# Kernel optimization log

Measured on AMD Instinct MI355X. Metric: run time of the kernel, lower is better.

The kernel has to match this reference:

```python
import jax, jax.numpy as jnp
import numpy as np

N = 100000
E = 3200000
D = 128
EPS = 1e-5


def setup_inputs() -> dict:
    key = jax.random.key(0)
    ks = jax.random.split(key, 9)
    h = jax.random.normal(ks[0], (N, D), dtype=jnp.float32)
    src = jax.random.randint(ks[1], (E,), 0, N, dtype=jnp.int64)
    dst = jax.random.randint(ks[2], (E,), 0, N, dtype=jnp.int64)
    s = 1.0 / np.sqrt(D)
    W_self = jax.random.uniform(ks[3], (D, D), jnp.float32, -s, s)
    W_neigh = jax.random.uniform(ks[4], (D, D), jnp.float32, -s, s)
    b = jax.random.uniform(ks[5], (D,), jnp.float32, -s, s)
    gamma = jnp.ones((D,), jnp.float32)
    beta = jnp.zeros((D,), jnp.float32)
    return {"h": h, "src": src, "dst": dst, "W_self": W_self,
            "W_neigh": W_neigh, "b": b, "gamma": gamma, "beta": beta}


def reference(h, src, dst, W_self, W_neigh, b, gamma, beta):
    # --- SAGEConv, mean aggregator (dropout p=0 -> identity) ---
    # gather source features along edges, segment-mean into destination nodes
    neigh_sum = jax.ops.segment_sum(h[src], dst, num_segments=N)      # [N, D]
    deg = jax.ops.segment_sum(jnp.ones((E,), h.dtype), dst, num_segments=N)
    neigh = neigh_sum / jnp.maximum(deg, 1.0)[:, None]                # [N, D]
    rst = h @ W_self + neigh @ W_neigh + b                            # [N, D]
    rst = jax.nn.relu(rst)                                            # activation
    # --- BatchNorm1d (training-mode batch statistics) ---
    mean = jnp.mean(rst, axis=0)
    var = jnp.var(rst, axis=0)
    rst = (rst - mean) * jax.lax.rsqrt(var + EPS) * gamma + beta
    # --- residual (in_feats == out_feats) ---
    return h + rst
```

## Files before the change

kernel.cpp:

```cpp
#include <hip/hip_runtime.h>

#define DCAP 2432
#define NBMAX 1600
#define SCATB 256
#define CONV2 512
#define WPB2 32
#define GB 1024
#define EORDCAP 3456

typedef __attribute__((ext_vector_type(2))) float f32x2;
typedef __attribute__((ext_vector_type(4))) float f32x4;
typedef __attribute__((ext_vector_type(8))) short bf16x8;

__device__ __forceinline__ unsigned short f2bf(float f) {
  union { float f; unsigned u; } c; c.f = f;
  unsigned u = c.u;
  unsigned r = u + 0x7FFFu + ((u >> 16) & 1u);
  return (unsigned short)(r >> 16);
}
__device__ __forceinline__ float bf2f(unsigned short s) {
  union { unsigned u; float f; } c; c.u = ((unsigned)s) << 16;
  return c.f;
}

__global__ __launch_bounds__(1024) void k_prescat(const float* __restrict__ h,
                                                  unsigned short* __restrict__ X,
                                                  unsigned* __restrict__ X8,
                                                  const float* __restrict__ Ws,
                                                  const float* __restrict__ Wn,
                                                  unsigned short* __restrict__ Wt,
                                                  const int* __restrict__ dst,
                                                  const int* __restrict__ src,
                                                  unsigned* __restrict__ esort,
                                                  int* __restrict__ gcur,
                                                  int nnodes, int E, int NB, int chunk) {
  __shared__ int cnt[NBMAX];
  __shared__ int gbase[NBMAX];
  int t = threadIdx.x;
  int bid = blockIdx.x;
  if (bid < SCATB) {
    int e0 = bid * chunk;
    int e1 = e0 + chunk; if (e1 > E) e1 = E;
    int n = e1 - e0;
    for (int i = t; i < NB; i += 1024) cnt[i] = 0;
    __syncthreads();
    for (int i = t; i < n; i += 1024)
      atomicAdd(&cnt[dst[e0 + i] >> 6], 1);
    __syncthreads();
    for (int bb = t; bb < NB; bb += 1024) {
      int len = cnt[bb];
      gbase[bb] = len ? atomicAdd(&gcur[bb], len) : 0;
      cnt[bb] = 0;
    }
    __syncthreads();
    for (int i = t; i < n; i += 1024) {
      int d = dst[e0 + i];
      int bb = d >> 6;
      int pos = gbase[bb] + atomicAdd(&cnt[bb], 1);
      if (pos < DCAP)
        esort[(long)bb * DCAP + pos] = ((unsigned)src[e0 + i] << 6) | (unsigned)(d & 63);
    }
  } else if (bid < SCATB + CONV2) {
    int stride = CONV2 * 1024;
    int total = nnodes * 32;
    for (int i = (bid - SCATB) * 1024 + t; i < total; i += stride) {
      int n = i >> 5, c = i & 31;
      float4 v = *(const float4*)(h + (long)n * 128 + c * 4);
      ushort4 o;
      o.x = f2bf(v.x); o.y = f2bf(v.y); o.z = f2bf(v.z); o.w = f2bf(v.w);
      *(ushort4*)(X + (long)n * 256 + c * 4) = o;
      int p8 = __builtin_amdgcn_cvt_pk_fp8_f32(v.x, v.y, 0, false);
      p8 = __builtin_amdgcn_cvt_pk_fp8_f32(v.z, v.w, p8, true);
      X8[(long)n * 32 + c] = (unsigned)p8;
    }
  } else if (bid < SCATB + CONV2 + WPB2) {
    int i = (bid - SCATB - CONV2) * 1024 + t;
    int col = i >> 8, k = i & 255;
    float v = (k < 128) ? Ws[k * 128 + col] : Wn[(k - 128) * 128 + col];
    Wt[col * 256 + k] = f2bf(v);
  } else {
    if (t < 32) X8[(long)nnodes * 32 + t] = 0u;
  }
}

__global__ __launch_bounds__(512) void k_aggb(unsigned short* __restrict__ X,
                                              const unsigned char* __restrict__ X8,
                                              const unsigned* __restrict__ esort,
                                              const int* __restrict__ gcur,
                                              int nnodes) {
  __shared__ unsigned eord[EORDCAP];
  __shared__ int dcnt[64], dstart[64], dcur[64], sc[64];
  int t = threadIdx.x;
  int b = blockIdx.x;
  int cntE = gcur[b]; if (cntE > DCAP) cntE = DCAP;
  const unsigned* ep = esort + (long)b * DCAP;
  if (t < 64) dcnt[t] = 0;
  __syncthreads();
  for (int i = t; i < cntE; i += 512)
    atomicAdd(&dcnt[ep[i] & 63u], 1);
  __syncthreads();
  int plen_t = 0;
  if (t < 64) { plen_t = (dcnt[t] + 15) & ~15; sc[t] = plen_t; }
  __syncthreads();
  for (int off = 1; off < 64; off <<= 1) {
    int v = (t < 64 && t >= off) ? sc[t - off] : 0;
    __syncthreads();
    if (t < 64) sc[t] += v;
    __syncthreads();
  }
  if (t < 64) { int ex = sc[t] - plen_t; dstart[t] = ex; dcur[t] = ex; }
  __syncthreads();
  int tot = sc[63];
  for (int i = t; i < tot; i += 512) eord[i] = (unsigned)nnodes;
  __syncthreads();
  for (int i = t; i < cntE; i += 512) {
    unsigned e = ep[i];
    int pos = atomicAdd(&dcur[e & 63u], 1);
    eord[pos] = e >> 6;
  }
  __syncthreads();

  int lane = t & 63, w = t >> 6;
  int qt = lane >> 4, ql = lane & 15;
  int ndst = nnodes - b * 64; if (ndst > 64) ndst = 64;
  for (int dl = w; dl < ndst; dl += 8) {
    int start = dstart[dl], dn = dcnt[dl];
    int plen = (dn + 15) & ~15;
    f32x2 acc[2][4];
#pragma unroll
    for (int u = 0; u < 2; u++)
#pragma unroll
      for (int j = 0; j < 4; j++) { acc[u][j].x = 0.f; acc[u][j].y = 0.f; }
    int i = 0;
    for (; i + 32 <= plen; i += 32) {
      uint2 v[8];
#pragma unroll
      for (int u = 0; u < 8; u++) {
        unsigned e = eord[start + i + u * 4 + qt];
        v[u] = *(const uint2*)(X8 + e * 128u + ql * 8u);
      }
#pragma unroll
      for (int u = 0; u < 8; u++) {
        acc[u & 1][0] += __builtin_amdgcn_cvt_pk_f32_fp8(v[u].x, false);
        acc[u & 1][1] += __builtin_amdgcn_cvt_pk_f32_fp8(v[u].x, true);
        acc[u & 1][2] += __builtin_amdgcn_cvt_pk_f32_fp8(v[u].y, false);
        acc[u & 1][3] += __builtin_amdgcn_cvt_pk_f32_fp8(v[u].y, true);
      }
    }
    if (i < plen) {
      uint2 v[4];
#pragma unroll
      for (int u = 0; u < 4; u++) {
        unsigned e = eord[start + i + u * 4 + qt];
        v[u] = *(const uint2*)(X8 + e * 128u + ql * 8u);
      }
#pragma unroll
      for (int u = 0; u < 4; u++) {
        acc[u & 1][0] += __builtin_amdgcn_cvt_pk_f32_fp8(v[u].x, false);
        acc[u & 1][1] += __builtin_amdgcn_cvt_pk_f32_fp8(v[u].x, true);
        acc[u & 1][2] += __builtin_amdgcn_cvt_pk_f32_fp8(v[u].y, false);
        acc[u & 1][3] += __builtin_amdgcn_cvt_pk_f32_fp8(v[u].y, true);
      }
    }
    float s[8];
#pragma unroll
    for (int j = 0; j < 4; j++) {
      s[2 * j] = acc[0][j].x + acc[1][j].x;
      s[2 * j + 1] = acc[0][j].y + acc[1][j].y;
    }
#pragma unroll
    for (int j = 0; j < 8; j++) {
      s[j] += __shfl_down(s[j], 32);
      s[j] += __shfl_down(s[j], 16);
    }
    if (qt == 0) {
      float scl = 1.0f / fmaxf((float)dn, 1.0f);
      uint4 o;
      o.x = (unsigned)f2bf(s[0] * scl) | ((unsigned)f2bf(s[1] * scl) << 16);
      o.y = (unsigned)f2bf(s[2] * scl) | ((unsigned)f2bf(s[3] * scl) << 16);
      o.z = (unsigned)f2bf(s[4] * scl) | ((unsigned)f2bf(s[5] * scl) << 16);
      o.w = (unsigned)f2bf(s[6] * scl) | ((unsigned)f2bf(s[7] * scl) << 16);
      *(uint4*)(X + (long)(b * 64 + dl) * 256 + 128 + ql * 8) = o;
    }
  }
}

__global__ __launch_bounds__(256) void k_gemm(const unsigned short* __restrict__ X,
                                              const unsigned short* __restrict__ Wt,
                                              const float* __restrict__ bias,
                                              unsigned short* __restrict__ rst8,
                                              float* __restrict__ psumA,
                                              float* __restrict__ psqA,
                                              int nnodes, int ntiles) {
  int t = threadIdx.x;
  int w = t >> 6, lane = t & 63;
  int m = lane & 15, q = lane >> 4;
  int col0 = w * 32 + m;
  int col1 = col0 + 16;
  bf16x8 b0[8], b1[8];
#pragma unroll
  for (int ks = 0; ks < 8; ks++) {
    b0[ks] = *(const bf16x8*)(Wt + col0 * 256 + q * 8 + ks * 32);
    b1[ks] = *(const bf16x8*)(Wt + col1 * 256 + q * 8 + ks * 32);
  }
  float bv0 = bias[col0], bv1 = bias[col1];
  float s0 = 0.f, sq0 = 0.f, s1 = 0.f, sq1 = 0.f;

#define LOADA(dst_, tb_)                                              \
  {                                                                   \
    int rowm_ = (tb_) * 16 + m;                                       \
    if (rowm_ >= nnodes) rowm_ = nnodes - 1;                          \
    const unsigned short* xp_ = X + (long)rowm_ * 256 + q * 8;        \
    _Pragma("unroll")                                                 \
    for (int ks = 0; ks < 8; ks++) dst_[ks] = *(const bf16x8*)(xp_ + ks * 32); \
  }

#define COMPUTE(a_, tb_)                                              \
  {                                                                   \
    f32x4 acc0 = {0.f, 0.f, 0.f, 0.f};                                \
    f32x4 acc1 = {0.f, 0.f, 0.f, 0.f};                                \
    _Pragma("unroll")                                                 \
    for (int ks = 0; ks < 8; ks++) {                                  \
      acc0 = __builtin_amdgcn_mfma_f32_16x16x32_bf16(a_[ks], b0[ks], acc0, 0, 0, 0); \
      acc1 = __builtin_amdgcn_mfma_f32_16x16x32_bf16(a_[ks], b1[ks], acc1, 0, 0, 0); \
    }                                                                 \
    _Pragma("unroll")                                                 \
    for (int r = 0; r < 4; r++) {                                     \
      int row = (tb_) * 16 + q * 4 + r;                               \
      if (row < nnodes) {                                             \
        float v0 = acc0[r] + bv0; v0 = v0 > 0.f ? v0 : 0.f;           \
        float v1 = acc1[r] + bv1; v1 = v1 > 0.f ? v1 : 0.f;           \
        rst8[(long)row * 128 + col0] = f2bf(v0);                      \
        rst8[(long)row * 128 + col1] = f2bf(v1);                      \
        s0 += v0; sq0 += v0 * v0;                                     \
        s1 += v1; sq1 += v1 * v1;                                     \
      }                                                               \
    }                                                                 \
  }

  int tb = blockIdx.x;
  if (tb < ntiles) {
    bf16x8 aA[8], aB[8];
    LOADA(aA, tb);
    for (; tb < ntiles; tb += 2 * GB) {
      int tb1 = tb + GB;
      if (tb1 < ntiles) LOADA(aB, tb1);
      COMPUTE(aA, tb);
      if (tb1 < ntiles) {
        int tb2 = tb1 + GB;
        if (tb2 < ntiles) LOADA(aA, tb2);
        COMPUTE(aB, tb1);
      }
    }
  }
#undef LOADA
#undef COMPUTE

  s0 += __shfl_down(s0, 32);  s0 += __shfl_down(s0, 16);
  sq0 += __shfl_down(sq0, 32); sq0 += __shfl_down(sq0, 16);
  s1 += __shfl_down(s1, 32);  s1 += __shfl_down(s1, 16);
  sq1 += __shfl_down(sq1, 32); sq1 += __shfl_down(sq1, 16);
  if (lane < 16) {
    atomicAdd(&psumA[col0], s0);
    atomicAdd(&psumA[col1], s1);
    atomicAdd(&psqA[col0], sq0);
    atomicAdd(&psqA[col1], sq1);
  }
}

__global__ void k_final(const unsigned short* __restrict__ X,
                        float* __restrict__ out,
                        const unsigned short* __restrict__ rst8,
                        const float* __restrict__ psumA,
                        const float* __restrict__ psqA,
                        const float* __restrict__ gamma,
                        const float* __restrict__ beta,
                        int nnodes, float Nf) {
  __shared__ float sc_s[128], sh_s[128];
  int t = threadIdx.x;
  if (t < 128) {
    float s = psumA[t], s2 = psqA[t];
    float mean = s / Nf;
    float var = s2 / Nf - mean * mean;
    float inv = rsqrtf(var + 1e-5f);
    float scv = gamma[t] * inv;
    sc_s[t] = scv;
    sh_s[t] = beta[t] - mean * scv;
  }
  __syncthreads();
  long stride = (long)gridDim.x * blockDim.x;
  long total = (long)nnodes * 16;
  for (long i = (long)blockIdx.x * blockDim.x + t; i < total; i += stride) {
    int c = (int)(i & 15);
    long row = i >> 4;
    uint4 rv = *(const uint4*)(rst8 + i * 8);
    uint4 hv = *(const uint4*)(X + row * 256 + c * 8);
    float4 sc0 = *(const float4*)(sc_s + c * 8);
    float4 sc1 = *(const float4*)(sc_s + c * 8 + 4);
    float4 sh0 = *(const float4*)(sh_s + c * 8);
    float4 sh1 = *(const float4*)(sh_s + c * 8 + 4);
    float4 o0, o1;
    o0.x = bf2f((unsigned short)(hv.x & 0xFFFFu)) + bf2f((unsigned short)(rv.x & 0xFFFFu)) * sc0.x + sh0.x;
    o0.y = bf2f((unsigned short)(hv.x >> 16))     + bf2f((unsigned short)(rv.x >> 16)) * sc0.y + sh0.y;
    o0.z = bf2f((unsigned short)(hv.y & 0xFFFFu)) + bf2f((unsigned short)(rv.y & 0xFFFFu)) * sc0.z + sh0.z;
    o0.w = bf2f((unsigned short)(hv.y >> 16))     + bf2f((unsigned short)(rv.y >> 16)) * sc0.w + sh0.w;
    o1.x = bf2f((unsigned short)(hv.z & 0xFFFFu)) + bf2f((unsigned short)(rv.z & 0xFFFFu)) * sc1.x + sh1.x;
    o1.y = bf2f((unsigned short)(hv.z >> 16))     + bf2f((unsigned short)(rv.z >> 16)) * sc1.y + sh1.y;
    o1.z = bf2f((unsigned short)(hv.w & 0xFFFFu)) + bf2f((unsigned short)(rv.w & 0xFFFFu)) * sc1.z + sh1.z;
    o1.w = bf2f((unsigned short)(hv.w >> 16))     + bf2f((unsigned short)(rv.w >> 16)) * sc1.w + sh1.w;
    *(float4*)(out + i * 8) = o0;
    *(float4*)(out + i * 8 + 4) = o1;
  }
}

extern "C" void kernel_launch(void* const* d_in, const int* in_sizes, int n_in,
                              void* d_out, int out_size, void* d_ws, size_t ws_size,
                              hipStream_t stream) {
  const float* h     = (const float*)d_in[0];
  const int*   src   = (const int*)d_in[1];
  const int*   dst   = (const int*)d_in[2];
  const float* Ws    = (const float*)d_in[3];
  const float* Wn    = (const float*)d_in[4];
  const float* bias  = (const float*)d_in[5];
  const float* gamma = (const float*)d_in[6];
  const float* beta  = (const float*)d_in[7];
  float* out = (float*)d_out;

  int nnodes = in_sizes[0] / 128;
  int E = in_sizes[1];
  int NB = (nnodes + 63) >> 6;
  int ntiles = (nnodes + 15) >> 4;
  int chunk = (E + SCATB - 1) / SCATB;

  char* ws = (char*)d_ws;
  size_t off = 0;
  unsigned short* X = (unsigned short*)(ws + off); off += (size_t)nnodes * 256 * 2;
  size_t off_alias = off;
  unsigned* X8 = (unsigned*)(ws + off);            off += (size_t)(nnodes + 1) * 128;
  unsigned* esort = (unsigned*)(ws + off);         off += (size_t)NB * DCAP * 4;
  unsigned short* rst8 = (unsigned short*)(ws + off_alias);
  unsigned short* Wt = (unsigned short*)(ws + off); off += 128 * 256 * 2;
  int* gcur = (int*)(ws + off);                    off += (size_t)NBMAX * 4;
  float* psumA = (float*)(ws + off);               off += 512;
  float* psqA = (float*)(ws + off);                off += 512;

  hipMemsetAsync(gcur, 0, (size_t)NBMAX * 4 + 1024, stream);
  k_prescat<<<SCATB + CONV2 + WPB2 + 1, 1024, 0, stream>>>(
      h, X, X8, Ws, Wn, Wt, dst, src, esort, gcur, nnodes, E, NB, chunk);
  k_aggb<<<NB, 512, 0, stream>>>(X, (const unsigned char*)X8, esort, gcur, nnodes);
  k_gemm<<<GB, 256, 0, stream>>>(X, Wt, bias, rst8, psumA, psqA, nnodes, ntiles);
  k_final<<<4096, 256, 0, stream>>>(X, out, rst8, psumA, psqA, gamma, beta,
                                    nnodes, (float)nnodes);
}
```

Before: 291.2 us.

## Replace global-atomic edge bucketing with per-chunk local sort and LDS-staged GEMM

Each scatter block now prefix-sums its local bucket counts. It writes edges into its own contiguous chunk of esort and records per-bucket counts and offsets in matrices, which removes the global atomic cursors and the memset. The aggregation block, now 256 threads, gathers its bucket's segments from all 256 chunks into LDS via a scan. The GEMM stages A tiles through a swizzled, double-buffered LDS tile instead of per-lane strided global loads. The cost is a serial, uncoalesced per-thread segment copy in aggregation, plus extra barriers and LDS use.

```diff
diff --git a/kernel.cpp b/kernel.cpp
--- a/kernel.cpp
+++ b/kernel.cpp
@@ -32,10 +32,12 @@
                                                   const int* __restrict__ dst,
                                                   const int* __restrict__ src,
                                                   unsigned* __restrict__ esort,
-                                                  int* __restrict__ gcur,
+                                                  int* __restrict__ cnt_mat,
+                                                  int* __restrict__ lofs_mat,
+                                                  float* __restrict__ psumA,
                                                   int nnodes, int E, int NB, int chunk) {
   __shared__ int cnt[NBMAX];
-  __shared__ int gbase[NBMAX];
+  __shared__ int tsum[1024];
   int t = threadIdx.x;
   int bid = blockIdx.x;
   if (bid < SCATB) {
@@ -47,18 +49,30 @@
     for (int i = t; i < n; i += 1024)
       atomicAdd(&cnt[dst[e0 + i] >> 6], 1);
     __syncthreads();
-    for (int bb = t; bb < NB; bb += 1024) {
-      int len = cnt[bb];
-      gbase[bb] = len ? atomicAdd(&gcur[bb], len) : 0;
-      cnt[bb] = 0;
+    int b0 = 2 * t, b1 = 2 * t + 1;
+    int c0 = (b0 < NB) ? cnt[b0] : 0;
+    int c1 = (b1 < NB) ? cnt[b1] : 0;
+    tsum[t] = c0 + c1;
+    __syncthreads();
+    for (int off = 1; off < 1024; off <<= 1) {
+      int v = (t >= off) ? tsum[t - off] : 0;
+      __syncthreads();
+      tsum[t] += v;
+      __syncthreads();
+    }
+    int ex = tsum[t] - (c0 + c1);
+    if (b0 < NB) {
+      *(int2*)&cnt_mat[(long)bid * NBMAX + b0] = make_int2(c0, c1);
+      *(int2*)&lofs_mat[(long)bid * NBMAX + b0] = make_int2(ex, ex + c0);
+      cnt[b0] = ex;
+      if (b1 < NB) cnt[b1] = ex + c0;
     }
     __syncthreads();
     for (int i = t; i < n; i += 1024) {
       int d = dst[e0 + i];
       int bb = d >> 6;
-      int pos = gbase[bb] + atomicAdd(&cnt[bb], 1);
-      if (pos < DCAP)
-        esort[(long)bb * DCAP + pos] = ((unsigned)src[e0 + i] << 6) | (unsigned)(d & 63);
+      int p = atomicAdd(&cnt[bb], 1);
+      esort[e0 + p] = ((unsigned)src[e0 + i] << 6) | (unsigned)(d & 63);
     }
   } else if (bid < SCATB + CONV2) {
     int stride = CONV2 * 1024;
@@ -80,24 +94,43 @@
     Wt[col * 256 + k] = f2bf(v);
   } else {
     if (t < 32) X8[(long)nnodes * 32 + t] = 0u;
-  }
-}
-
-__global__ __launch_bounds__(512) void k_aggb(unsigned short* __restrict__ X,
+    if (t >= 64 && t < 320) psumA[t - 64] = 0.f;
+  }
+}
+
+__global__ __launch_bounds__(256) void k_aggb(unsigned short* __restrict__ X,
                                               const unsigned char* __restrict__ X8,
                                               const unsigned* __restrict__ esort,
-                                              const int* __restrict__ gcur,
-                                              int nnodes) {
+                                              const int* __restrict__ cnt_mat,
+                                              const int* __restrict__ lofs_mat,
+                                              int nnodes, int chunk) {
+  __shared__ unsigned eload[DCAP];
   __shared__ unsigned eord[EORDCAP];
+  __shared__ int sseg[256];
   __shared__ int dcnt[64], dstart[64], dcur[64], sc[64];
   int t = threadIdx.x;
   int b = blockIdx.x;
-  int cntE = gcur[b]; if (cntE > DCAP) cntE = DCAP;
-  const unsigned* ep = esort + (long)b * DCAP;
+  int len = cnt_mat[(long)t * NBMAX + b];
+  int lof = lofs_mat[(long)t * NBMAX + b];
+  sseg[t] = len;
+  __syncthreads();
+  for (int off = 1; off < 256; off <<= 1) {
+    int v = (t >= off) ? sseg[t - off] : 0;
+    __syncthreads();
+    sseg[t] += v;
+    __syncthreads();
+  }
+  int dsto = sseg[t] - len;
+  int cntE = sseg[255]; if (cntE > DCAP) cntE = DCAP;
+  const unsigned* sp = esort + (long)t * chunk + lof;
+  for (int j = 0; j < len; j++) {
+    int di = dsto + j;
+    if (di < DCAP) eload[di] = sp[j];
+  }
   if (t < 64) dcnt[t] = 0;
   __syncthreads();
-  for (int i = t; i < cntE; i += 512)
-    atomicAdd(&dcnt[ep[i] & 63u], 1);
+  for (int i = t; i < cntE; i += 256)
+    atomicAdd(&dcnt[eload[i] & 63u], 1);
   __syncthreads();
   int plen_t = 0;
   if (t < 64) { plen_t = (dcnt[t] + 15) & ~15; sc[t] = plen_t; }
@@ -111,10 +144,10 @@
   if (t < 64) { int ex = sc[t] - plen_t; dstart[t] = ex; dcur[t] = ex; }
   __syncthreads();
   int tot = sc[63];
-  for (int i = t; i < tot; i += 512) eord[i] = (unsigned)nnodes;
-  __syncthreads();
-  for (int i = t; i < cntE; i += 512) {
-    unsigned e = ep[i];
+  for (int i = t; i < tot; i += 256) eord[i] = (unsigned)nnodes;
+  __syncthreads();
+  for (int i = t; i < cntE; i += 256) {
+    unsigned e = eload[i];
     int pos = atomicAdd(&dcur[e & 63u], 1);
     eord[pos] = e >> 6;
   }
@@ -123,7 +156,7 @@
   int lane = t & 63, w = t >> 6;
   int qt = lane >> 4, ql = lane & 15;
   int ndst = nnodes - b * 64; if (ndst > 64) ndst = 64;
-  for (int dl = w; dl < ndst; dl += 8) {
+  for (int dl = w; dl < ndst; dl += 4) {
     int start = dstart[dl], dn = dcnt[dl];
     int plen = (dn + 15) & ~15;
     f32x2 acc[2][4];
@@ -192,6 +225,7 @@
                                               float* __restrict__ psumA,
                                               float* __restrict__ psqA,
                                               int nnodes, int ntiles) {
+  __shared__ unsigned short atile[2][16][256];
   int t = threadIdx.x;
   int w = t >> 6, lane = t & 63;
   int m = lane & 15, q = lane >> 4;
@@ -206,55 +240,53 @@
   float bv0 = bias[col0], bv1 = bias[col1];
   float s0 = 0.f, sq0 = 0.f, s1 = 0.f, sq1 = 0.f;
 
-#define LOADA(dst_, tb_)                                              \
-  {                                                                   \
-    int rowm_ = (tb_) * 16 + m;                                       \
-    if (rowm_ >= nnodes) rowm_ = nnodes - 1;                          \
-    const unsigned short* xp_ = X + (long)rowm_ * 256 + q * 8;        \
-    _Pragma("unroll")                                                 \
-    for (int ks = 0; ks < 8; ks++) dst_[ks] = *(const bf16x8*)(xp_ + ks * 32); \
-  }
-
-#define COMPUTE(a_, tb_)                                              \
-  {                                                                   \
-    f32x4 acc0 = {0.f, 0.f, 0.f, 0.f};                                \
-    f32x4 acc1 = {0.f, 0.f, 0.f, 0.f};                                \
-    _Pragma("unroll")                                                 \
-    for (int ks = 0; ks < 8; ks++) {                                  \
-      acc0 = __builtin_amdgcn_mfma_f32_16x16x32_bf16(a_[ks], b0[ks], acc0, 0, 0, 0); \
-      acc1 = __builtin_amdgcn_mfma_f32_16x16x32_bf16(a_[ks], b1[ks], acc1, 0, 0, 0); \
-    }                                                                 \
-    _Pragma("unroll")                                                 \
-    for (int r = 0; r < 4; r++) {                                     \
-      int row = (tb_) * 16 + q * 4 + r;                               \
-      if (row < nnodes) {                                             \
-        float v0 = acc0[r] + bv0; v0 = v0 > 0.f ? v0 : 0.f;           \
-        float v1 = acc1[r] + bv1; v1 = v1 > 0.f ? v1 : 0.f;           \
-        rst8[(long)row * 128 + col0] = f2bf(v0);                      \
-        rst8[(long)row * 128 + col1] = f2bf(v1);                      \
-        s0 += v0; sq0 += v0 * v0;                                     \
-        s1 += v1; sq1 += v1 * v1;                                     \
-      }                                                               \
-    }                                                                 \
+#define STAGE(bufi, tb_)                                                        \
+  {                                                                             \
+    int r_ = t >> 4;                                                            \
+    long row_ = (long)(tb_) * 16 + r_;                                          \
+    if (row_ >= nnodes) row_ = nnodes - 1;                                      \
+    const unsigned short* gp_ = X + row_ * 256 + (t & 15) * 16;                 \
+    uint4 d0_ = *(const uint4*)gp_;                                             \
+    uint4 d1_ = *(const uint4*)(gp_ + 8);                                       \
+    int bo_ = (t & 15) * 32;                                                    \
+    char* lb_ = (char*)&atile[bufi][0][0] + r_ * 512;                           \
+    *(uint4*)(lb_ + (bo_ ^ ((r_ & 7) << 4))) = d0_;                             \
+    *(uint4*)(lb_ + ((bo_ + 16) ^ ((r_ & 7) << 4))) = d1_;                      \
   }
 
   int tb = blockIdx.x;
-  if (tb < ntiles) {
-    bf16x8 aA[8], aB[8];
-    LOADA(aA, tb);
-    for (; tb < ntiles; tb += 2 * GB) {
-      int tb1 = tb + GB;
-      if (tb1 < ntiles) LOADA(aB, tb1);
-      COMPUTE(aA, tb);
-      if (tb1 < ntiles) {
-        int tb2 = tb1 + GB;
-        if (tb2 < ntiles) LOADA(aA, tb2);
-        COMPUTE(aB, tb1);
-      }
-    }
-  }
-#undef LOADA
-#undef COMPUTE
+  int it = 0;
+  if (tb < ntiles) STAGE(0, tb);
+  for (; tb < ntiles; tb += GB, ++it) {
+    __syncthreads();
+    const char* lb = (const char*)&atile[it & 1][0][0] + m * 512;
+    bf16x8 a[8];
+#pragma unroll
+    for (int ks = 0; ks < 8; ks++)
+      a[ks] = *(const bf16x8*)(lb + ((q * 16 + ks * 64) ^ ((m & 7) << 4)));
+    int tbn = tb + GB;
+    if (tbn < ntiles) STAGE((it + 1) & 1, tbn);
+    f32x4 acc0 = {0.f, 0.f, 0.f, 0.f};
+    f32x4 acc1 = {0.f, 0.f, 0.f, 0.f};
+#pragma unroll
+    for (int ks = 0; ks < 8; ks++) {
+      acc0 = __builtin_amdgcn_mfma_f32_16x16x32_bf16(a[ks], b0[ks], acc0, 0, 0, 0);
+      acc1 = __builtin_amdgcn_mfma_f32_16x16x32_bf16(a[ks], b1[ks], acc1, 0, 0, 0);
+    }
+#pragma unroll
+    for (int r = 0; r < 4; r++) {
+      int row = tb * 16 + q * 4 + r;
+      if (row < nnodes) {
+        float v0 = acc0[r] + bv0; v0 = v0 > 0.f ? v0 : 0.f;
+        float v1 = acc1[r] + bv1; v1 = v1 > 0.f ? v1 : 0.f;
+        rst8[(long)row * 128 + col0] = f2bf(v0);
+        rst8[(long)row * 128 + col1] = f2bf(v1);
+        s0 += v0; sq0 += v0 * v0;
+        s1 += v1; sq1 += v1 * v1;
+      }
+    }
+  }
+#undef STAGE
 
   s0 += __shfl_down(s0, 32);  s0 += __shfl_down(s0, 16);
   sq0 += __shfl_down(sq0, 32); sq0 += __shfl_down(sq0, 16);
@@ -337,17 +369,19 @@
   unsigned short* X = (unsigned short*)(ws + off); off += (size_t)nnodes * 256 * 2;
   size_t off_alias = off;
   unsigned* X8 = (unsigned*)(ws + off);            off += (size_t)(nnodes + 1) * 128;
-  unsigned* esort = (unsigned*)(ws + off);         off += (size_t)NB * DCAP * 4;
+  unsigned* esort = (unsigned*)(ws + off);         off += (size_t)(E + 1024) * 4;
   unsigned short* rst8 = (unsigned short*)(ws + off_alias);
   unsigned short* Wt = (unsigned short*)(ws + off); off += 128 * 256 * 2;
-  int* gcur = (int*)(ws + off);                    off += (size_t)NBMAX * 4;
   float* psumA = (float*)(ws + off);               off += 512;
   float* psqA = (float*)(ws + off);                off += 512;
-
-  hipMemsetAsync(gcur, 0, (size_t)NBMAX * 4 + 1024, stream);
+  int* cnt_mat = (int*)(ws + off);                 off += (size_t)SCATB * NBMAX * 4;
+  int* lofs_mat = (int*)(ws + off);                off += (size_t)SCATB * NBMAX * 4;
+
   k_prescat<<<SCATB + CONV2 + WPB2 + 1, 1024, 0, stream>>>(
-      h, X, X8, Ws, Wn, Wt, dst, src, esort, gcur, nnodes, E, NB, chunk);
-  k_aggb<<<NB, 512, 0, stream>>>(X, (const unsigned char*)X8, esort, gcur, nnodes);
+      h, X, X8, Ws, Wn, Wt, dst, src, esort, cnt_mat, lofs_mat, psumA,
+      nnodes, E, NB, chunk);
+  k_aggb<<<NB, 256, 0, stream>>>(X, (const unsigned char*)X8, esort, cnt_mat,
+                                 lofs_mat, nnodes, chunk);
   k_gemm<<<GB, 256, 0, stream>>>(X, Wt, bias, rst8, psumA, psqA, nnodes, ntiles);
   k_final<<<4096, 256, 0, stream>>>(X, out, rst8, psumA, psqA, gamma, beta,
                                     nnodes, (float)nnodes);
```

Measured after the change: 298.2 us. 1.02x slower.
